# Kernel optimization log

Measured on AMD Instinct MI355X. Metric: run time of the kernel, lower is better.

The kernel has to match this reference:

```python
import jax, jax.numpy as jnp
import numpy as np

KR = 2  # nb_row == stride_row
KC = 2  # nb_col == stride_col


def setup_inputs() -> dict:
    key = jax.random.key(0)
    k1, k2, k3 = jax.random.split(key, 3)
    B, C, H, W_ = 32, 32, 128, 128
    F = 64
    OR, OC = H // KR, W_ // KC
    x = jax.random.normal(k1, (B, C, H, W_), dtype=jnp.float32)
    W = jax.random.normal(k2, (F, C, H, W_), dtype=jnp.float32) * 0.05
    b = jax.random.normal(k3, (OR, OC, F), dtype=jnp.float32) * 0.05
    return {"x": x, "W": W, "b": b}


def reference(x, W, b):
    # x: (B, C, H, W), W: (F, C, H, W) -- unshared per-pixel weights
    # per-pixel channel contraction: (B, F, H, W)
    out = jnp.einsum('bchw,fchw->bfhw', x, W)
    B, F, H, Wd = out.shape
    OR, OC = H // KR, Wd // KC
    # stride*avg_pool == exact sum over non-overlapping (KR, KC) patches
    out = out.reshape(B, F, OR, KR, OC, KC).sum(axis=(3, 5))
    # keras does a RAW reshape of b from (OR, OC, F) to (1, F, OR, OC)
    out = out + b.reshape(1, F, OR, OC)
    return jax.nn.relu(out)
```

## Files before the change

kernel.cpp:

```cpp
#include <hip/hip_runtime.h>
#include <stdint.h>


#define CC  32
#define HH  128
#define WWD 128
#define FF  64
#define ORR 64
#define OCC 64
#define CB  2
#define NIT (CC / CB)
#define CSTRIDE (CB * HH * WWD)

#define XBUF 4096
#define WBUF 8192

__global__ __launch_bounds__(1024, 4) void lc2d_kernel(
    const float* __restrict__ x, const float* __restrict__ wgt,
    const float* __restrict__ bias, float* __restrict__ out)
{
    __shared__ __align__(16) float Xs[2][XBUF];
    __shared__ __align__(16) float Ws[2][WBUF];

    const int tid = threadIdx.x;
    const int id  = blockIdx.x;
    const int oct = ((id & 1) << 1) | (id >> 7);
    const int orr = (id >> 1) & 63;
    const int w0  = oct * 32;
    const int h0  = orr * 2;

    const int lane = tid & 63;
    const int wv   = tid >> 6;
    const int chk  = lane & 7;
    const int sub  = lane >> 3;

    int r  = wv * 8 + sub;
    const float* gx  = x   + (((((r & 31) * CC) + (r >> 6)) * HH) + h0 + ((r >> 5) & 1)) * WWD + w0 + chk * 4;
    int r0 = wv * 8 + sub;
    const float* gw0 = wgt + (((((r0 & 63) * CC) + (r0 >> 7)) * HH) + h0 + ((r0 >> 6) & 1)) * WWD + w0 + chk * 4;
    int r1 = (wv + 16) * 8 + sub;
    const float* gw1 = wgt + (((((r1 & 63) * CC) + (r1 >> 7)) * HH) + h0 + ((r1 >> 6) & 1)) * WWD + w0 + chk * 4;

    auto issue = [&](int p) {
        __builtin_amdgcn_global_load_lds(
            (const __attribute__((address_space(1))) void*)gx,
            (__attribute__((address_space(3))) void*)(&Xs[p][wv * 256]), 16, 0, 0);
        __builtin_amdgcn_global_load_lds(
            (const __attribute__((address_space(1))) void*)gw0,
            (__attribute__((address_space(3))) void*)(&Ws[p][wv * 256]), 16, 0, 0);
        __builtin_amdgcn_global_load_lds(
            (const __attribute__((address_space(1))) void*)gw1,
            (__attribute__((address_space(3))) void*)(&Ws[p][4096 + wv * 256]), 16, 0, 0);
        gx += CSTRIDE; gw0 += CSTRIDE; gw1 += CSTRIDE;
    };

    issue(0);
    issue(1);

    const int ocg = tid & 7;
    const int bg  = (tid >> 3) & 7;
    const int fg  = wv;
    const int xoff = bg * 128 + ocg * 4;
    const int woff = fg * 128 + ocg * 4;

    float acc0[4][4], acc1[4][4];
#pragma unroll
    for (int i = 0; i < 4; ++i)
#pragma unroll
        for (int q = 0; q < 4; ++q) { acc0[i][q] = 0.f; acc1[i][q] = 0.f; }

    for (int it = 0; it < NIT; ++it) {
        const int p = it & 1;
        if (it == NIT - 1) __builtin_amdgcn_s_waitcnt(0x0F70);
        else               __builtin_amdgcn_s_waitcnt(0x0F73);
        __syncthreads();

        const float* Xp = Xs[p];
        const float* Wp = Ws[p];
#pragma unroll
        for (int s = 0; s < 2 * CB; ++s) {
            const float4* xr = (const float4*)(Xp + s * 1024 + xoff);
            const float4* wr = (const float4*)(Wp + s * 2048 + woff);
            float4 xa[4], wa[4];
#pragma unroll
            for (int i = 0; i < 4; ++i) xa[i] = xr[i * 8];
#pragma unroll
            for (int q = 0; q < 4; ++q) wa[q] = wr[q * 8];
#pragma unroll
            for (int i = 0; i < 4; ++i)
#pragma unroll
                for (int q = 0; q < 4; ++q) {
                    acc0[i][q] = fmaf(xa[i].x, wa[q].x, acc0[i][q]);
                    acc0[i][q] = fmaf(xa[i].y, wa[q].y, acc0[i][q]);
                    acc1[i][q] = fmaf(xa[i].z, wa[q].z, acc1[i][q]);
                    acc1[i][q] = fmaf(xa[i].w, wa[q].w, acc1[i][q]);
                }
        }
        __syncthreads();
        if (it + 2 < NIT) issue(p);
    }

    const int oc0 = oct * 16 + ocg * 2;
#pragma unroll
    for (int q = 0; q < 4; ++q) {
        const int f = fg * 4 + q;
        const float2 bv = *(const float2*)(bias + f * (ORR * OCC) + orr * OCC + oc0);
#pragma unroll
        for (int i = 0; i < 4; ++i) {
            const int b = bg * 4 + i;
            float2 o;
            o.x = fmaxf(acc0[i][q] + bv.x, 0.f);
            o.y = fmaxf(acc1[i][q] + bv.y, 0.f);
            *(float2*)(out + (((b * FF + f) * ORR + orr) * OCC) + oc0) = o;
        }
    }
}

extern "C" void kernel_launch(void* const* d_in, const int* in_sizes, int n_in,
                              void* d_out, int out_size, void* d_ws, size_t ws_size,
                              hipStream_t stream) {
    (void)in_sizes; (void)n_in; (void)d_ws; (void)ws_size; (void)out_size;
    const float* x    = (const float*)d_in[0];
    const float* wgt  = (const float*)d_in[1];
    const float* bias = (const float*)d_in[2];
    float* out        = (float*)d_out;
    lc2d_kernel<<<dim3(256, 1, 1), dim3(1024, 1, 1), 0, stream>>>(x, wgt, bias, out);
}
```

Before: 289.4 us.

## Restructure double-buffer pipeline to one barrier per step with prefetch depth one

Replaces the two-ahead prefetch with two __syncthreads per iteration by a one-ahead prefetch. After waiting for all outstanding loads, each step runs a single barrier with LDS fences, then issues the next buffer's loads before computing. The loop is unrolled by two so the buffer pointers are compile-time constants. This halves barrier count, but each step now stalls until its loads land, so load latency is less hidden than with two tiles in flight.

```diff
diff --git a/kernel.cpp b/kernel.cpp
--- a/kernel.cpp
+++ b/kernel.cpp
@@ -41,21 +41,18 @@
     int r1 = (wv + 16) * 8 + sub;
     const float* gw1 = wgt + (((((r1 & 63) * CC) + (r1 >> 7)) * HH) + h0 + ((r1 >> 6) & 1)) * WWD + w0 + chk * 4;
 
-    auto issue = [&](int p) {
+    auto issue = [&](float* xb, float* wb) {
         __builtin_amdgcn_global_load_lds(
             (const __attribute__((address_space(1))) void*)gx,
-            (__attribute__((address_space(3))) void*)(&Xs[p][wv * 256]), 16, 0, 0);
+            (__attribute__((address_space(3))) void*)(xb + wv * 256), 16, 0, 0);
         __builtin_amdgcn_global_load_lds(
             (const __attribute__((address_space(1))) void*)gw0,
-            (__attribute__((address_space(3))) void*)(&Ws[p][wv * 256]), 16, 0, 0);
+            (__attribute__((address_space(3))) void*)(wb + wv * 256), 16, 0, 0);
         __builtin_amdgcn_global_load_lds(
             (const __attribute__((address_space(1))) void*)gw1,
-            (__attribute__((address_space(3))) void*)(&Ws[p][4096 + wv * 256]), 16, 0, 0);
+            (__attribute__((address_space(3))) void*)(wb + 4096 + wv * 256), 16, 0, 0);
         gx += CSTRIDE; gw0 += CSTRIDE; gw1 += CSTRIDE;
     };
-
-    issue(0);
-    issue(1);
 
     const int ocg = tid & 7;
     const int bg  = (tid >> 3) & 7;
@@ -69,14 +66,15 @@
 #pragma unroll
         for (int q = 0; q < 4; ++q) { acc0[i][q] = 0.f; acc1[i][q] = 0.f; }
 
-    for (int it = 0; it < NIT; ++it) {
-        const int p = it & 1;
-        if (it == NIT - 1) __builtin_amdgcn_s_waitcnt(0x0F70);
-        else               __builtin_amdgcn_s_waitcnt(0x0F73);
-        __syncthreads();
+    issue(&Xs[0][0], &Ws[0][0]);
 
-        const float* Xp = Xs[p];
-        const float* Wp = Ws[p];
+    auto kstep = [&](int it, const float* Xp, const float* Wp, float* Xn, float* Wn) {
+        __builtin_amdgcn_s_waitcnt(0x0F70);
+        __builtin_amdgcn_fence(__ATOMIC_ACQ_REL, "workgroup", "local");
+        __builtin_amdgcn_s_barrier();
+        __builtin_amdgcn_fence(__ATOMIC_ACQ_REL, "workgroup", "local");
+        if (it + 1 < NIT) issue(Xn, Wn);
+
 #pragma unroll
         for (int s = 0; s < 2 * CB; ++s) {
             const float4* xr = (const float4*)(Xp + s * 1024 + xoff);
@@ -96,8 +94,12 @@
                     acc1[i][q] = fmaf(xa[i].w, wa[q].w, acc1[i][q]);
                 }
         }
-        __syncthreads();
-        if (it + 2 < NIT) issue(p);
+    };
+
+#pragma unroll 1
+    for (int it = 0; it < NIT; it += 2) {
+        kstep(it,     &Xs[0][0], &Ws[0][0], &Xs[1][0], &Ws[1][0]);
+        kstep(it + 1, &Xs[1][0], &Ws[1][0], &Xs[0][0], &Ws[0][0]);
     }
 
     const int oc0 = oct * 16 + ocg * 2;
```

New measurement: 430.5 us. 48.8% more time.
